# Kernel tuning notes

Hardware: AMD Instinct MI355X
Metric: run time of the kernel (lower is better)

Reference implementation:

```python
import jax, jax.numpy as jnp
import numpy as np


def gat(feat_src, feat_dst, src, dst, W, al, ar, b):
    # DGL GATConv in eval mode: shared fc for src/dst, additive attention,
    # leaky_relu(0.2), edge-softmax per destination node, elu activation, bias.
    H, D = al.shape
    nd = feat_dst.shape[0]
    hs = (feat_src @ W).reshape(-1, H, D)  # [Ns,H,D]
    hd = (feat_dst @ W).reshape(-1, H, D)  # [Nd,H,D]
    el = (hs * al).sum(-1)  # [Ns,H]
    er = (hd * ar).sum(-1)  # [Nd,H]
    e = jax.nn.leaky_relu(el[src] + er[dst], 0.2)  # [E,H]
    m = jax.lax.stop_gradient(jax.ops.segment_max(e, dst, num_segments=nd))
    a = jnp.exp(e - m[dst])
    s = jax.ops.segment_sum(a, dst, num_segments=nd)
    den = s[dst]
    alpha = a / jnp.where(den == 0, 1.0, den)  # allow_zero_in_degree
    rst = jax.ops.segment_sum(alpha[:, :, None] * hs[src], dst, num_segments=nd)
    return jax.nn.elu(rst + b.reshape(H, D))  # [Nd,H,D]


def setup_inputs():
    key = jax.random.key(0)
    ks = jax.random.split(key, 40)
    NP, NQ, NK, NA = 50000, 20000, 30000, 5000
    EM, EQ, EK, EA = 1600000, 200000, 200000, 100000
    IN, ATT, HID, H, OUT = 128, 64, 32, 4, 1000
    w = lambda k, sh: jax.random.normal(k, sh, jnp.float32) * 0.05
    ri = lambda k, e, n: jax.random.randint(k, (e,), 0, n, dtype=jnp.int32)
    d = dict(
        hp=jax.random.normal(ks[0], (NP, IN), jnp.float32),
        hq=jax.random.normal(ks[1], (NQ, ATT), jnp.float32),
        hk=jax.random.normal(ks[2], (NK, ATT), jnp.float32),
        ha=jax.random.normal(ks[3], (NA, ATT), jnp.float32),
        meta_src=ri(ks[4], EM, NP), meta_dst=ri(ks[5], EM, NP),
        q_src=ri(ks[6], EQ, NQ), q_dst=ri(ks[7], EQ, NP),
        k_src=ri(ks[8], EK, NK), k_dst=ri(ks[9], EK, NP),
        a_src=ri(ks[10], EA, NA), a_dst=ri(ks[11], EA, NP),
        W0=w(ks[12], (IN, H * HID)), al0=w(ks[13], (H, HID)), ar0=w(ks[14], (H, HID)), b0=jnp.zeros((H * HID,), jnp.float32),
        W1=w(ks[15], (H * HID, H * HID)), al1=w(ks[16], (H, HID)), ar1=w(ks[17], (H, HID)), b1=jnp.zeros((H * HID,), jnp.float32),
        Wq=w(ks[18], (64, H * 128)), alq=w(ks[19], (H, 128)), arq=w(ks[20], (H, 128)), bq=jnp.zeros((H * 128,), jnp.float32),
        Wkw=w(ks[21], (64, H * 128)), alkw=w(ks[22], (H, 128)), arkw=w(ks[23], (H, 128)), bkw=jnp.zeros((H * 128,), jnp.float32),
        Watt=w(ks[24], (64, H * 128)), alatt=w(ks[25], (H, 128)), aratt=w(ks[26], (H, 128)), batt=jnp.zeros((H * 128,), jnp.float32),
        Wpnn_a=w(ks[27], (IN, 64)), Wpn_a=w(ks[28], (ATT, 64)),
        Wpnn=w(ks[29], (H * HID, 64)), Wpn=w(ks[30], (H * 128, 64)),
        Wpred=w(ks[31], (256, OUT)), bpred=jnp.zeros((OUT,), jnp.float32),
    )
    return d


def reference(hp, hq, hk, ha, meta_src, meta_dst, q_src, q_dst, k_src, k_dst, a_src, a_dst, W0, al0, ar0, b0, W1, al1, ar1, b1, Wq, alq, arq, bq, Wkw, alkw, arkw, bkw, Watt, alatt, aratt, batt, Wpnn_a, Wpn_a, Wpnn, Wpn, Wpred, bpred):
    NP = hp.shape[0]
    # two pnn_layers over the single used metapath graph (index 1 is skipped in the original)
    h = gat(hp, hp, meta_src, meta_dst, W0, al0, ar0, b0).reshape(NP, -1)  # [NP,128]
    h = gat(h, h, meta_src, meta_dst, W1, al1, ar1, b1).reshape(NP, -1)    # [NP,128]
    hpd = hp @ Wpnn_a  # proj_pnn_a(hp_cache) -> dst features for bipartite GATs
    oq = gat(hq @ Wpn_a, hpd, q_src, q_dst, Wq, alq, arq, bq).reshape(NP, -1)      # [NP,512]
    ok = gat(hk @ Wpn_a, hpd, k_src, k_dst, Wkw, alkw, arkw, bkw).reshape(NP, -1)  # [NP,512]
    oa = gat(ha @ Wpn_a, hpd, a_src, a_dst, Watt, alatt, aratt, batt).reshape(NP, -1)  # [NP,512]
    hcat = jnp.concatenate([h @ Wpnn, oq @ Wpn, ok @ Wpn, oa @ Wpn], axis=1)  # [NP,256]
    return hcat @ Wpred + bpred
```

## Files before the change

### kernel.cpp

```cpp
#include <hip/hip_runtime.h>
#include <hip/hip_bf16.h>
#include <math.h>
#include <stdint.h>

typedef __attribute__((ext_vector_type(8))) short bh8;
typedef __attribute__((ext_vector_type(4))) float f32x4;

#define AS1(p) ((const __attribute__((address_space(1))) void*)(p))
#define AS3(p) ((__attribute__((address_space(3))) void*)(p))

__device__ inline ushort f2b(float f){
  uint u = __builtin_bit_cast(uint, f);
  u += 0x7fff + ((u >> 16) & 1);
  return (ushort)(u >> 16);
}
__device__ inline float b2f(ushort b){ return __builtin_bit_cast(float, (uint)b << 16); }

__global__ void fill_zero_i32(int* __restrict__ p, int n){
  int i = blockIdx.x*blockDim.x + threadIdx.x;
  if(i < n) p[i] = 0;
}

struct P4 { const int* src; const int* dst; uint* ebuf; int E; int cap; int bbeg; int bend; };

__global__ __launch_bounds__(256) void partition_all_k(P4 g0, P4 g1, P4 g2, P4 g3,
    int* __restrict__ bcur, int range){
  P4 G; int gi;
  int b = blockIdx.x;
  if(b < g0.bend){ G = g0; gi = 0; }
  else if(b < g1.bend){ G = g1; gi = 1; }
  else if(b < g2.bend){ G = g2; gi = 2; }
  else { G = g3; gi = 3; }
  const int lb = b - G.bbeg, nb = G.bend - G.bbeg;
  __shared__ int hist[8], base[8];
  const int tid = threadIdx.x;
  int* bc = bcur + gi*8;
  for(int c0 = lb*256; c0 < G.E; c0 += nb*256){
    int i = c0 + tid;
    int d = 0, s = 0, bk = -1;
    if(i < G.E){ d = G.dst[i]; s = G.src[i]; bk = d / range; }
    if(tid < 8) hist[tid] = 0;
    __syncthreads();
    int rank = 0;
    if(bk >= 0) rank = atomicAdd(&hist[bk], 1);
    __syncthreads();
    if(tid < 8) base[tid] = hist[tid] ? atomicAdd(&bc[tid], hist[tid]) : 0;
    __syncthreads();
    if(bk >= 0){
      int pos = base[bk] + rank;
      if(pos < G.cap) G.ebuf[(size_t)bk*G.cap + pos] = ((uint)s << 13) | (uint)(d - bk*range);
    }
    __syncthreads();
  }
}

struct B4 { const uint* ebuf; int cap; int* cnt; int bbeg; int bend; };
__global__ __launch_bounds__(256) void count_all_k(B4 g0, B4 g1, B4 g2, B4 g3,
    const int* __restrict__ bcur, int range){
  B4 G; int gi;
  int b = blockIdx.x;
  if(b < g0.bend){ G = g0; gi = 0; }
  else if(b < g1.bend){ G = g1; gi = 1; }
  else if(b < g2.bend){ G = g2; gi = 2; }
  else { G = g3; gi = 3; }
  const int local = b - G.bbeg, J = (G.bend - G.bbeg) >> 3;
  const int bk = local & 7, j = local >> 3;
  int nb = bcur[gi*8 + bk]; if(nb > G.cap) nb = G.cap;
  const uint* eb = G.ebuf + (size_t)bk*G.cap;
  int* cb = G.cnt + bk*range;
  int per = (nb + J - 1)/J;
  int beg = j*per, end = beg + per; if(end > nb) end = nb;
  for(int i = beg + threadIdx.x; i < end; i += 256)
    atomicAdd(&cb[eb[i] & 8191u], 1);
}

struct SB4 { const uint* ebuf; int cap; int* cursor; int* colv; int bbeg; int bend; };
__global__ __launch_bounds__(256) void scatter_all_k(SB4 g0, SB4 g1, SB4 g2, SB4 g3,
    const int* __restrict__ bcur, int range){
  SB4 G; int gi;
  int b = blockIdx.x;
  if(b < g0.bend){ G = g0; gi = 0; }
  else if(b < g1.bend){ G = g1; gi = 1; }
  else if(b < g2.bend){ G = g2; gi = 2; }
  else { G = g3; gi = 3; }
  const int local = b - G.bbeg, J = (G.bend - G.bbeg) >> 3;
  const int bk = local & 7, j = local >> 3;
  int nb = bcur[gi*8 + bk]; if(nb > G.cap) nb = G.cap;
  const uint* eb = G.ebuf + (size_t)bk*G.cap;
  int* ub = G.cursor + bk*range;
  int per = (nb + J - 1)/J;
  int beg = j*per, end = beg + per; if(end > nb) end = nb;
  for(int i = beg + threadIdx.x; i < end; i += 256){
    uint e = eb[i];
    int p = atomicAdd(&ub[e & 8191u], 1);
    G.colv[p] = (int)(e >> 13);
  }
}

__global__ __launch_bounds__(1024) void scan4_k(
    const int* c0, const int* c1, const int* c2, const int* c3,
    int* o0, int* o1, int* o2, int* o3,
    int* u0, int* u1, int* u2, int* u3, int n){
  const int* cnt = blockIdx.x==0?c0:(blockIdx.x==1?c1:(blockIdx.x==2?c2:c3));
  int* ofs    = blockIdx.x==0?o0:(blockIdx.x==1?o1:(blockIdx.x==2?o2:o3));
  int* cursor = blockIdx.x==0?u0:(blockIdx.x==1?u1:(blockIdx.x==2?u2:u3));
  __shared__ int wsum[16];
  __shared__ int carry_s;
  int tid = threadIdx.x, wid = tid >> 6, lane = tid & 63;
  if(tid == 0) carry_s = 0;
  __syncthreads();
  for(int base = 0; base < n; base += 4096){
    int i0 = base + tid*4;
    int4 v = make_int4(0,0,0,0);
    if(i0 + 3 < n) v = *(const int4*)(cnt + i0);
    else if(i0 < n){
      v.x = cnt[i0];
      if(i0+1 < n) v.y = cnt[i0+1];
      if(i0+2 < n) v.z = cnt[i0+2];
    }
    int s1 = v.x + v.y, s2 = s1 + v.z, tot = s2 + v.w;
    int x = tot;
    #pragma unroll
    for(int off = 1; off < 64; off <<= 1){
      int t = __shfl_up(x, off);
      if(lane >= off) x += t;
    }
    if(lane == 63) wsum[wid] = x;
    __syncthreads();
    if(tid < 16){
      int y = wsum[tid];
      #pragma unroll
      for(int off = 1; off < 16; off <<= 1){
        int t = __shfl_up(y, off);
        if(tid >= off) y += t;
      }
      wsum[tid] = y;
    }
    __syncthreads();
    int pre = (wid ? wsum[wid-1] : 0) + carry_s + (x - tot);
    if(i0 + 3 < n){
      int4 o = make_int4(pre, pre+v.x, pre+s1, pre+s2);
      *(int4*)(ofs + i0) = o;
      *(int4*)(cursor + i0) = o;
    } else if(i0 < n){
      ofs[i0] = pre; cursor[i0] = pre;
      if(i0+1 < n){ ofs[i0+1] = pre+v.x; cursor[i0+1] = pre+v.x; }
      if(i0+2 < n){ ofs[i0+2] = pre+s1; cursor[i0+2] = pre+s1; }
    }
    __syncthreads();
    if(tid == 0) carry_s += wsum[15];
    __syncthreads();
  }
  if(tid == 0) ofs[n] = carry_s;
}

__global__ void cvt_all_k(const float* i0, const float* i1, const float* i2, const float* i3,
    ushort* o0, ushort* o1, ushort* o2, ushort* o3, int4 cum){
  int i = blockIdx.x*blockDim.x + threadIdx.x;
  const float* in; ushort* out; int base;
  if(i < cum.x){ in=i0; out=o0; base=0; }
  else if(i < cum.y){ in=i1; out=o1; base=cum.x; }
  else if(i < cum.z){ in=i2; out=o2; base=cum.y; }
  else if(i < cum.w){ in=i3; out=o3; base=cum.z; }
  else return;
  int l = i - base;
  float4 v = ((const float4*)in)[l];
  ushort4 o; o.x=f2b(v.x); o.y=f2b(v.y); o.z=f2b(v.z); o.w=f2b(v.w);
  ((ushort4*)out)[l] = o;
}

struct WTD { const float* W; ushort* WT; int K; int N; };
struct WTAll { WTD d[7]; int cum[8]; };
__global__ void wT_all_k(WTAll a){
  int idx = blockIdx.x*blockDim.x + threadIdx.x;
  if(idx >= a.cum[7]) return;
  int j = 0;
  #pragma unroll
  for(int t = 1; t < 7; t++) if(idx >= a.cum[t]) j = t;
  int l = idx - a.cum[j];
  WTD d = a.d[j];
  int n = l / d.K, k = l - n*d.K;
  d.WT[l] = (n < d.N) ? f2b(d.W[(size_t)k*d.N + n]) : (ushort)0;
}

__global__ void wTg3_k(const float* W0, const float* W1, const float* W2, ushort* WT){
  int idx = blockIdx.x*blockDim.x + threadIdx.x;
  if(idx >= 3*32768) return;
  int g = idx >> 15, rem = idx & 32767;
  const float* W = g==0 ? W0 : (g==1 ? W1 : W2);
  int h = rem >> 13, r2 = rem & 8191;
  int n = r2 >> 6, k = r2 & 63;
  WT[idx] = f2b(W[(size_t)k*512 + h*128 + n]);
}

struct FD { const float* W; const float* a; float* out; int K; int D; };
struct FAll { FD d[10]; };
__global__ void fold_all_k(FAll f){
  FD d = f.d[blockIdx.x];
  for(int i = threadIdx.x; i < d.K*4; i += 256){
    int k = i >> 2, h = i & 3;
    const float* wr = d.W + (size_t)k*4*d.D + (size_t)h*d.D;
    const float* ar = d.a + (size_t)h*d.D;
    float s = 0.f;
    for(int dd = 0; dd < d.D; dd++) s += wr[dd]*ar[dd];
    d.out[i] = s;
  }
}

__device__ inline void ld4v(const float* p, float* v){
  float4 t = *(const float4*)p; v[0]=t.x; v[1]=t.y; v[2]=t.z; v[3]=t.w;
}
__device__ inline void ld4v(const ushort* p, float* v){
  ushort4 t = *(const ushort4*)p; v[0]=b2f(t.x); v[1]=b2f(t.y); v[2]=b2f(t.z); v[3]=b2f(t.w);
}

__global__ __launch_bounds__(256) void gemv4v_seg3(const ushort* __restrict__ A,
    const float* __restrict__ W0, const float* __restrict__ W1, const float* __restrict__ W2,
    float* __restrict__ outv, int M, int b1, int b2){
  const int w = (blockIdx.x*blockDim.x + threadIdx.x) >> 6;
  const int lane = threadIdx.x & 63;
  const int r = lane >> 4, q = lane & 15;
  int row = w*4 + r;
  bool valid = row < M;
  int rowc = valid ? row : (M-1);
  const float* Wf = rowc < b1 ? W0 : (rowc < b2 ? W1 : W2);
  float av[4];
  ld4v(A + (size_t)rowc*64 + q*4, av);
  float a[4] = {0.f,0.f,0.f,0.f};
  #pragma unroll
  for(int kk = 0; kk < 4; kk++){
    float4 wv = *(const float4*)(Wf + (q*4+kk)*4);
    a[0] += av[kk]*wv.x; a[1] += av[kk]*wv.y; a[2] += av[kk]*wv.z; a[3] += av[kk]*wv.w;
  }
  #pragma unroll
  for(int off = 1; off < 16; off <<= 1){
    a[0] += __shfl_xor(a[0], off); a[1] += __shfl_xor(a[1], off);
    a[2] += __shfl_xor(a[2], off); a[3] += __shfl_xor(a[3], off);
  }
  if(valid && q == 0){
    float4 o; o.x=a[0]; o.y=a[1]; o.z=a[2]; o.w=a[3];
    *(float4*)(outv + (size_t)row*4) = o;
  }
}

__global__ __launch_bounds__(256) void gemv4v_er3(const ushort* __restrict__ A,
    const float* __restrict__ W0, const float* __restrict__ W1, const float* __restrict__ W2,
    float* __restrict__ o0, float* __restrict__ o1, float* __restrict__ o2, int M){
  const int w = (blockIdx.x*blockDim.x + threadIdx.x) >> 6;
  const int lane = threadIdx.x & 63;
  const int r = lane >> 4, q = lane & 15;
  int row = w*4 + r;
  bool valid = row < M;
  int rowc = valid ? row : (M-1);
  float av[4];
  ld4v(A + (size_t)rowc*64 + q*4, av);
  float a[12];
  #pragma unroll
  for(int t = 0; t < 12; t++) a[t] = 0.f;
  #pragma unroll
  for(int kk = 0; kk < 4; kk++){
    float4 w0 = *(const float4*)(W0 + (q*4+kk)*4);
    float4 w1 = *(const float4*)(W1 + (q*4+kk)*4);
    float4 w2 = *(const float4*)(W2 + (q*4+kk)*4);
    a[0] += av[kk]*w0.x; a[1] += av[kk]*w0.y; a[2] += av[kk]*w0.z; a[3] += av[kk]*w0.w;
    a[4] += av[kk]*w1.x; a[5] += av[kk]*w1.y; a[6] += av[kk]*w1.z; a[7] += av[kk]*w1.w;
    a[8] += av[kk]*w2.x; a[9] += av[kk]*w2.y; a[10]+= av[kk]*w2.z; a[11]+= av[kk]*w2.w;
  }
  #pragma unroll
  for(int off = 1; off < 16; off <<= 1)
    #pragma unroll
    for(int t = 0; t < 12; t++) a[t] += __shfl_xor(a[t], off);
  if(valid && q == 0){
    float4 x; x.x=a[0]; x.y=a[1]; x.z=a[2]; x.w=a[3];
    *(float4*)(o0 + (size_t)row*4) = x;
    float4 y; y.x=a[4]; y.y=a[5]; y.z=a[6]; y.w=a[7];
    *(float4*)(o1 + (size_t)row*4) = y;
    float4 z; z.x=a[8]; z.y=a[9]; z.z=a[10]; z.w=a[11];
    *(float4*)(o2 + (size_t)row*4) = z;
  }
}

template<typename T>
__global__ __launch_bounds__(256) void gemv8v(const T* __restrict__ A,
    const float* __restrict__ Wfa, const float* __restrict__ Wfb,
    float* __restrict__ oa, float* __restrict__ ob, int M, int lda){
  const int w = (blockIdx.x*blockDim.x + threadIdx.x) >> 6;
  const int lane = threadIdx.x & 63;
  const int r = lane >> 5, q = lane & 31;
  int row = w*2 + r;
  bool valid = row < M;
  int rowc = valid ? row : (M-1);
  float av[4];
  ld4v(A + (size_t)rowc*lda + q*4, av);
  float a[4] = {0.f,0.f,0.f,0.f}, b[4] = {0.f,0.f,0.f,0.f};
  #pragma unroll
  for(int kk = 0; kk < 4; kk++){
    float4 wa = *(const float4*)(Wfa + (q*4+kk)*4);
    float4 wb = *(const float4*)(Wfb + (q*4+kk)*4);
    a[0] += av[kk]*wa.x; a[1] += av[kk]*wa.y; a[2] += av[kk]*wa.z; a[3] += av[kk]*wa.w;
    b[0] += av[kk]*wb.x; b[1] += av[kk]*wb.y; b[2] += av[kk]*wb.z; b[3] += av[kk]*wb.w;
  }
  #pragma unroll
  for(int off = 1; off < 32; off <<= 1){
    a[0] += __shfl_xor(a[0], off); a[1] += __shfl_xor(a[1], off);
    a[2] += __shfl_xor(a[2], off); a[3] += __shfl_xor(a[3], off);
    b[0] += __shfl_xor(b[0], off); b[1] += __shfl_xor(b[1], off);
    b[2] += __shfl_xor(b[2], off); b[3] += __shfl_xor(b[3], off);
  }
  if(valid && q == 0){
    float4 o; o.x=a[0]; o.y=a[1]; o.z=a[2]; o.w=a[3];
    *(float4*)(oa + (size_t)row*4) = o;
    float4 p; p.x=b[0]; p.y=b[1]; p.z=b[2]; p.w=b[3];
    *(float4*)(ob + (size_t)row*4) = p;
  }
}

struct GSeg { const ushort* A; const ushort* BT; const float* bias; void* C; int ldc; };

template<int BN, typename OutT, bool BIAS>
__global__ __launch_bounds__(256) void gemm_mfma_b(GSeg s0, GSeg s1, GSeg s2,
    int M, int N, int K, int lda){
  constexpr int BM = 128, BK = 64;
  constexpr int NI = BN/32;
  constexpr int AIT = BM*BK/(256*8);
  constexpr int BIT = BN*BK/(256*8);
  __shared__ ushort lds[BM*BK + BN*BK];
  ushort* ldsA = lds;
  ushort* ldsB = lds + BM*BK;
  GSeg S = blockIdx.z == 0 ? s0 : (blockIdx.z == 1 ? s1 : s2);
  const int tid = threadIdx.x, wid = tid >> 6, lane = tid & 63;
  const int wr = wid >> 1, wc = wid & 1;
  const int rowbase = blockIdx.x*BM;
  const int colbase = blockIdx.y*BN;

  f32x4 acc[4][NI];
  #pragma unroll
  for(int mi = 0; mi < 4; mi++)
    #pragma unroll
    for(int ni = 0; ni < NI; ni++) acc[mi][ni] = (f32x4)0.f;

  for(int k0 = 0; k0 < K; k0 += BK){
    #pragma unroll
    for(int it = 0; it < AIT; it++){
      int idx = it*256 + wid*64 + lane;
      int r = idx >> 3, sl = idx & 7;
      int kb = sl ^ (r & 7);
      int grow = rowbase + r; if(grow >= M) grow = M-1;
      const ushort* src = S.A + (size_t)grow*lda + k0 + kb*8;
      __builtin_amdgcn_global_load_lds(AS1(src), AS3(ldsA + (size_t)(it*256 + wid*64)*8), 16, 0, 0);
    }
    #pragma unroll
    for(int it = 0; it < BIT; it++){
      int idx = it*256 + wid*64 + lane;
      int r = idx >> 3, sl = idx & 7;
      int kb = sl ^ (r & 7);
      const ushort* src = S.BT + (size_t)(colbase + r)*K + k0 + kb*8;
      __builtin_amdgcn_global_load_lds(AS1(src), AS3(ldsB + (size_t)(it*256 + wid*64)*8), 16, 0, 0);
    }
    __syncthreads();
    #pragma unroll
    for(int kk = 0; kk < 2; kk++){
      bh8 af[4], bf[NI];
      #pragma unroll
      for(int mi = 0; mi < 4; mi++){
        int arow = wr*64 + mi*16 + (lane & 15);
        int kb = kk*4 + (lane >> 4);
        af[mi] = *(const bh8*)(ldsA + arow*BK + ((kb ^ (arow & 7)) << 3));
      }
      #pragma unroll
      for(int ni = 0; ni < NI; ni++){
        int brow = wc*(BN/2) + ni*16 + (lane & 15);
        int kb = kk*4 + (lane >> 4);
        bf[ni] = *(const bh8*)(ldsB + brow*BK + ((kb ^ (brow & 7)) << 3));
      }
      #pragma unroll
      for(int mi = 0; mi < 4; mi++)
        #pragma unroll
        for(int ni = 0; ni < NI; ni++)
          acc[mi][ni] = __builtin_amdgcn_mfma_f32_16x16x32_bf16(af[mi], bf[ni], acc[mi][ni], 0, 0, 0);
    }
    __syncthreads();
  }
  OutT* C = (OutT*)S.C;
  #pragma unroll
  for(int mi = 0; mi < 4; mi++){
    #pragma unroll
    for(int ni = 0; ni < NI; ni++){
      int col = colbase + wc*(BN/2) + ni*16 + (lane & 15);
      if(col >= N) continue;
      float bv = BIAS ? S.bias[col] : 0.f;
      #pragma unroll
      for(int j = 0; j < 4; j++){
        int row = rowbase + wr*64 + mi*16 + (lane >> 4)*4 + j;
        if(row >= M) continue;
        float v = acc[mi][ni][j] + bv;
        if constexpr (sizeof(OutT) == 4) C[(size_t)row*S.ldc + col] = v;
        else                             C[(size_t)row*S.ldc + col] = (OutT)f2b(v);
      }
    }
  }
}

__global__ __launch_bounds__(256) void bip_tail_k(
    const ushort* __restrict__ agg,
    const ushort* __restrict__ WTg3,
    const ushort* __restrict__ WpnT,
    const float* bias0, const float* bias1, const float* bias2,
    ushort* __restrict__ hcat,
    int M){
  __shared__ ushort ldsA[128*64];
  __shared__ ushort ldsB[128*64];
  __shared__ ushort ldsP[128*128];
  __shared__ ushort ldsW[64*128];
  const int seg = blockIdx.z;
  const ushort* A  = agg + (size_t)seg*M*256;
  const ushort* Wg = WTg3 + (size_t)seg*32768;
  const float* bias = seg==0 ? bias0 : (seg==1 ? bias1 : bias2);
  ushort* outp = hcat + 64 + seg*64;
  const int tid = threadIdx.x, lane = tid & 63, wid = tid >> 6;
  const int wr = wid >> 1, wc = wid & 1;
  const int rowbase = blockIdx.x*128;

  f32x4 acc_out[4][2];
  #pragma unroll
  for(int mi = 0; mi < 4; mi++){ acc_out[mi][0] = (f32x4)0.f; acc_out[mi][1] = (f32x4)0.f; }

  for(int hh = 0; hh < 4; hh++){
    #pragma unroll
    for(int it = 0; it < 4; it++){
      int idx = it*256 + tid;
      int r = idx >> 3, sl = idx & 7;
      int kb = sl ^ (r & 7);
      int grow = rowbase + r; if(grow >= M) grow = M-1;
      __builtin_amdgcn_global_load_lds(AS1(A + (size_t)grow*256 + hh*64 + kb*8),
                                       AS3(ldsA + (size_t)idx*8), 16, 0, 0);
    }
    #pragma unroll
    for(int it = 0; it < 4; it++){
      int idx = it*256 + tid;
      int r = idx >> 3, sl = idx & 7;
      int kb = sl ^ (r & 7);
      __builtin_amdgcn_global_load_lds(AS1(Wg + hh*8192 + r*64 + kb*8),
                                       AS3(ldsB + (size_t)idx*8), 16, 0, 0);
    }
    #pragma unroll
    for(int it = 0; it < 4; it++){
      int idx = it*256 + tid;
      int r = idx >> 4, sl = idx & 15;
      int kb = sl ^ (r & 7);
      __builtin_amdgcn_global_load_lds(AS1(WpnT + (size_t)r*512 + hh*128 + kb*8),
                                       AS3(ldsW + (size_t)idx*8), 16, 0, 0);
    }
    __syncthreads();
    f32x4 accp[4][4];
    #pragma unroll
    for(int mi = 0; mi < 4; mi++)
      #pragma unroll
      for(int ni = 0; ni < 4; ni++) accp[mi][ni] = (f32x4)0.f;
    #pragma unroll
    for(int kk = 0; kk < 2; kk++){
      bh8 af[4], bf[4];
      int kb = kk*4 + (lane >> 4);
      #pragma unroll
      for(int mi = 0; mi < 4; mi++){
        int arow = wr*64 + mi*16 + (lane & 15);
        af[mi] = *(const bh8*)(ldsA + arow*64 + ((kb ^ (arow & 7)) << 3));
      }
      #pragma unroll
      for(int ni = 0; ni < 4; ni++){
        int brow = wc*64 + ni*16 + (lane & 15);
        bf[ni] = *(const bh8*)(ldsB + brow*64 + ((kb ^ (brow & 7)) << 3));
      }
      #pragma unroll
      for(int mi = 0; mi < 4; mi++)
        #pragma unroll
        for(int ni = 0; ni < 4; ni++)
          accp[mi][ni] = __builtin_amdgcn_mfma_f32_16x16x32_bf16(af[mi], bf[ni], accp[mi][ni], 0, 0, 0);
    }
    #pragma unroll
    for(int mi = 0; mi < 4; mi++)
      #pragma unroll
      for(int ni = 0; ni < 4; ni++){
        int col = wc*64 + ni*16 + (lane & 15);
        float bv = bias[hh*128 + col];
        int rbase = wr*64 + mi*16 + (lane >> 4)*4;
        #pragma unroll
        for(int j = 0; j < 4; j++){
          float v = accp[mi][ni][j] + bv;
          v = v > 0.f ? v : (__expf(v) - 1.f);
          int row = rbase + j;
          ldsP[row*128 + ((((col >> 3) ^ (row & 7))) << 3) + (col & 7)] = f2b(v);
        }
      }
    __syncthreads();
    #pragma unroll
    for(int kk = 0; kk < 4; kk++){
      bh8 af[4], bf[2];
      int kb = kk*4 + (lane >> 4);
      #pragma unroll
      for(int mi = 0; mi < 4; mi++){
        int arow = wr*64 + mi*16 + (lane & 15);
        af[mi] = *(const bh8*)(ldsP + arow*128 + ((kb ^ (arow & 7)) << 3));
      }
      #pragma unroll
      for(int ni = 0; ni < 2; ni++){
        int brow = wc*32 + ni*16 + (lane & 15);
        bf[ni] = *(const bh8*)(ldsW + brow*128 + ((kb ^ (brow & 7)) << 3));
      }
      #pragma unroll
      for(int mi = 0; mi < 4; mi++)
        #pragma unroll
        for(int ni = 0; ni < 2; ni++)
          acc_out[mi][ni] = __builtin_amdgcn_mfma_f32_16x16x32_bf16(af[mi], bf[ni], acc_out[mi][ni], 0, 0, 0);
    }
    __syncthreads();
  }
  #pragma unroll
  for(int mi = 0; mi < 4; mi++)
    #pragma unroll
    for(int ni = 0; ni < 2; ni++){
      int col = wc*32 + ni*16 + (lane & 15);
      #pragma unroll
      for(int j = 0; j < 4; j++){
        int row = rowbase + wr*64 + mi*16 + (lane >> 4)*4 + j;
        if(row >= M) continue;
        outp[(size_t)row*256 + col] = f2b(acc_out[mi][ni][j]);
      }
    }
}

__global__ __launch_bounds__(256) void gat_agg_meta(
    const ushort* __restrict__ hs, const float* __restrict__ el,
    const float* __restrict__ er, const int* __restrict__ ofs,
    const int* __restrict__ colv, const float* __restrict__ bias,
    ushort* __restrict__ outv, int Nd){
  const int wslot = threadIdx.x >> 6;
  const int node = blockIdx.x*4 + wslot;
  const int lane = threadIdx.x & 63;
  __shared__ int   lds_s[4][64];
  __shared__ float lds_w[4][256];
  if(node >= Nd) return;
  const int e0 = ofs[node], e1 = ofs[node+1];
  const int g = lane >> 4, q = lane & 15;
  const int hh = q >> 2;
  const float4 erv = *(const float4*)(er + (size_t)node*4);
  float m0=-INFINITY, m1=-INFINITY, m2=-INFINITY, m3=-INFINITY;
  float sw0=0.f, sw1=0.f, sw2=0.f, sw3=0.f;
  float acc[8];
  #pragma unroll
  for(int r = 0; r < 8; r++) acc[r] = 0.f;

  for(int base = e0; base < e1; base += 64){
    int nch = e1 - base; if(nch > 64) nch = 64;
    int s_l = colv[base + (lane < nch ? lane : nch-1)];
    float4 ev = *(const float4*)(el + (size_t)s_l*4);
    float x0 = ev.x + erv.x; x0 = x0 > 0.f ? x0 : 0.2f*x0;
    float x1 = ev.y + erv.y; x1 = x1 > 0.f ? x1 : 0.2f*x1;
    float x2 = ev.z + erv.z; x2 = x2 > 0.f ? x2 : 0.2f*x2;
    float x3 = ev.w + erv.w; x3 = x3 > 0.f ? x3 : 0.2f*x3;
    if(lane >= nch){ x0 = x1 = x2 = x3 = -INFINITY; }
    float c0=x0, c1=x1, c2=x2, c3=x3;
    #pragma unroll
    for(int off = 32; off; off >>= 1){
      c0 = fmaxf(c0, __shfl_xor(c0, off));
      c1 = fmaxf(c1, __shfl_xor(c1, off));
      c2 = fmaxf(c2, __shfl_xor(c2, off));
      c3 = fmaxf(c3, __shfl_xor(c3, off));
    }
    float n0 = fmaxf(m0,c0), n1 = fmaxf(m1,c1), n2 = fmaxf(m2,c2), n3 = fmaxf(m3,c3);
    float r0 = __expf(m0-n0), r1 = __expf(m1-n1), r2 = __expf(m2-n2), r3 = __expf(m3-n3);
    float w0 = __expf(x0-n0), w1 = __expf(x1-n1), w2 = __expf(x2-n2), w3 = __expf(x3-n3);
    sw0 = sw0*r0 + w0; sw1 = sw1*r1 + w1; sw2 = sw2*r2 + w2; sw3 = sw3*r3 + w3;
    float rh = hh==0 ? r0 : (hh==1 ? r1 : (hh==2 ? r2 : r3));
    #pragma unroll
    for(int r = 0; r < 8; r++) acc[r] *= rh;
    m0=n0; m1=n1; m2=n2; m3=n3;
    lds_s[wslot][lane] = s_l;
    lds_w[wslot][lane*4+0] = w0; lds_w[wslot][lane*4+1] = w1;
    lds_w[wslot][lane*4+2] = w2; lds_w[wslot][lane*4+3] = w3;
    int npad = (nch + 7) & ~7;
    for(int j = 0; j < npad; j += 8){
      int sA = lds_s[wslot][j + g];
      int sB = lds_s[wslot][j + 4 + g];
      float wA = lds_w[wslot][(j + g)*4 + hh];
      float wB = lds_w[wslot][(j + 4 + g)*4 + hh];
      bh8 vA = *(const bh8*)(hs + (size_t)sA*128 + q*8);
      bh8 vB = *(const bh8*)(hs + (size_t)sB*128 + q*8);
      #pragma unroll
      for(int r = 0; r < 8; r++) acc[r] += wA * b2f((ushort)vA[r]);
      #pragma unroll
      for(int r = 0; r < 8; r++) acc[r] += wB * b2f((ushort)vB[r]);
    }
  }
  #pragma unroll
  for(int off = 32; off; off >>= 1){
    sw0 += __shfl_xor(sw0, off); sw1 += __shfl_xor(sw1, off);
    sw2 += __shfl_xor(sw2, off); sw3 += __shfl_xor(sw3, off);
  }
  #pragma unroll
  for(int r = 0; r < 8; r++){
    acc[r] += __shfl_xor(acc[r], 16);
    acc[r] += __shfl_xor(acc[r], 32);
  }
  float swh = hh==0 ? sw0 : (hh==1 ? sw1 : (hh==2 ? sw2 : sw3));
  float den = (swh == 0.f) ? 1.f : swh;
  if(g == 0){
    bh8 ov;
    #pragma unroll
    for(int r = 0; r < 8; r++){
      float v = acc[r]/den + bias[q*8 + r];
      v = v > 0.f ? v : (__expf(v) - 1.f);
      ov[r] = (short)f2b(v);
    }
    *(bh8*)(outv + (size_t)node*128 + q*8) = ov;
  }
}

struct ASeg { const int* ofs; const int* colv; const float* el; const float* er; ushort* agg; };
__global__ __launch_bounds__(256) void gat_agg_proj3(ASeg s0, ASeg s1, ASeg s2,
    const ushort* __restrict__ proj, int2 pbase, int Nd, int nb){
  const int seg = blockIdx.x / nb;
  const ASeg S = seg == 0 ? s0 : (seg == 1 ? s1 : s2);
  const ushort* pj = proj + (size_t)(seg == 0 ? 0 : (seg == 1 ? pbase.x : pbase.y))*64;
  const int node = (blockIdx.x - seg*nb)*16 + (threadIdx.x >> 4);
  const int q = threadIdx.x & 15;
  if(node >= Nd) return;
  const int e0 = S.ofs[node], e1 = S.ofs[node+1];
  const float4 erv = *(const float4*)(S.er + (size_t)node*4);
  float m0=-INFINITY, m1=-INFINITY, m2=-INFINITY, m3=-INFINITY;
  for(int e = e0; e < e1; e++){
    int s = S.colv[e];
    float4 ev = *(const float4*)(S.el + (size_t)s*4);
    float x0 = ev.x + erv.x; x0 = x0 > 0.f ? x0 : 0.2f*x0;
    float x1 = ev.y + erv.y; x1 = x1 > 0.f ? x1 : 0.2f*x1;
    float x2 = ev.z + erv.z; x2 = x2 > 0.f ? x2 : 0.2f*x2;
    float x3 = ev.w + erv.w; x3 = x3 > 0.f ? x3 : 0.2f*x3;
    m0 = fmaxf(m0,x0); m1 = fmaxf(m1,x1); m2 = fmaxf(m2,x2); m3 = fmaxf(m3,x3);
  }
  float sw0=0.f, sw1=0.f, sw2=0.f, sw3=0.f;
  float acc[4][4];
  #pragma unroll
  for(int d = 0; d < 4; d++)
    #pragma unroll
    for(int h = 0; h < 4; h++) acc[d][h] = 0.f;
  for(int e = e0; e < e1; e++){
    int s = S.colv[e];
    float4 ev = *(const float4*)(S.el + (size_t)s*4);
    float x0 = ev.x + erv.x; x0 = x0 > 0.f ? x0 : 0.2f*x0;
    float x1 = ev.y + erv.y; x1 = x1 > 0.f ? x1 : 0.2f*x1;
    float x2 = ev.z + erv.z; x2 = x2 > 0.f ? x2 : 0.2f*x2;
    float x3 = ev.w + erv.w; x3 = x3 > 0.f ? x3 : 0.2f*x3;
    float w0 = __expf(x0-m0), w1 = __expf(x1-m1);
    float w2 = __expf(x2-m2), w3 = __expf(x3-m3);
    sw0 += w0; sw1 += w1; sw2 += w2; sw3 += w3;
    ushort4 p = *(const ushort4*)(pj + (size_t)s*64 + q*4);
    float f0 = b2f(p.x), f1 = b2f(p.y), f2 = b2f(p.z), f3 = b2f(p.w);
    acc[0][0] += w0*f0; acc[0][1] += w1*f0; acc[0][2] += w2*f0; acc[0][3] += w3*f0;
    acc[1][0] += w0*f1; acc[1][1] += w1*f1; acc[1][2] += w2*f1; acc[1][3] += w3*f1;
    acc[2][0] += w0*f2; acc[2][1] += w1*f2; acc[2][2] += w2*f2; acc[2][3] += w3*f2;
    acc[3][0] += w0*f3; acc[3][1] += w1*f3; acc[3][2] += w2*f3; acc[3][3] += w3*f3;
  }
  float dn[4];
  dn[0] = (sw0 == 0.f) ? 1.f : sw0;
  dn[1] = (sw1 == 0.f) ? 1.f : sw1;
  dn[2] = (sw2 == 0.f) ? 1.f : sw2;
  dn[3] = (sw3 == 0.f) ? 1.f : sw3;
  ushort* orow = S.agg + (size_t)node*256;
  #pragma unroll
  for(int h = 0; h < 4; h++){
    ushort4 o;
    o.x = f2b(acc[0][h]/dn[h]); o.y = f2b(acc[1][h]/dn[h]);
    o.z = f2b(acc[2][h]/dn[h]); o.w = f2b(acc[3][h]/dn[h]);
    *(ushort4*)(orow + h*64 + q*4) = o;
  }
}

extern "C" void kernel_launch(void* const* d_in, const int* in_sizes, int n_in,
                              void* d_out, int out_size, void* d_ws, size_t ws_size,
                              hipStream_t stream){
  const float* hp   = (const float*)d_in[0];
  const float* hq   = (const float*)d_in[1];
  const float* hk   = (const float*)d_in[2];
  const float* ha   = (const float*)d_in[3];
  const int* meta_src = (const int*)d_in[4];
  const int* meta_dst = (const int*)d_in[5];
  const int* q_src = (const int*)d_in[6];
  const int* q_dst = (const int*)d_in[7];
  const int* k_src = (const int*)d_in[8];
  const int* k_dst = (const int*)d_in[9];
  const int* a_src = (const int*)d_in[10];
  const int* a_dst = (const int*)d_in[11];
  const float* W0  = (const float*)d_in[12]; const float* al0 = (const float*)d_in[13];
  const float* ar0 = (const float*)d_in[14]; const float* b0  = (const float*)d_in[15];
  const float* W1  = (const float*)d_in[16]; const float* al1 = (const float*)d_in[17];
  const float* ar1 = (const float*)d_in[18]; const float* b1  = (const float*)d_in[19];
  const float* Wq  = (const float*)d_in[20]; const float* alq = (const float*)d_in[21];
  const float* arq = (const float*)d_in[22]; const float* bq  = (const float*)d_in[23];
  const float* Wkw = (const float*)d_in[24]; const float* alkw= (const float*)d_in[25];
  const float* arkw= (const float*)d_in[26]; const float* bkw = (const float*)d_in[27];
  const float* Watt= (const float*)d_in[28]; const float* alatt=(const float*)d_in[29];
  const float* aratt=(const float*)d_in[30]; const float* batt= (const float*)d_in[31];
  const float* Wpnn_a = (const float*)d_in[32];
  const float* Wpn_a  = (const float*)d_in[33];
  const float* Wpnn   = (const float*)d_in[34];
  const float* Wpn    = (const float*)d_in[35];
  const float* Wpred  = (const float*)d_in[36];
  const float* bpred  = (const float*)d_in[37];
  (void)n_in; (void)out_size; (void)ws_size;

  const int IN = 128, ATT = 64;
  const int NP = in_sizes[0]/IN, NQ = in_sizes[1]/ATT, NK = in_sizes[2]/ATT, NA = in_sizes[3]/ATT;
  const int EM = in_sizes[4], EQ = in_sizes[6], EK = in_sizes[8], EA = in_sizes[10];
  const int range = (NP + 7)/8;
  const int NS = NQ + NK + NA;

  uint8_t* wp = (uint8_t*)d_ws;
  auto alloc = [&](size_t bytes)->uint8_t*{
    uint8_t* p = wp; wp += (bytes + 255) & ~(size_t)255; return p;
  };
  ushort* hcat_b = (ushort*)alloc((size_t)NP*256*2);
  ushort* hbuf_b = (ushort*)alloc((size_t)NP*128*2);
  ushort* hp_b   = (ushort*)alloc((size_t)NP*128*2);
  ushort* hpd_b  = (ushort*)alloc((size_t)NP*64*2);
  ushort* hs_b   = (ushort*)alloc((size_t)NP*128*2);
  ushort* feat_all = (ushort*)alloc((size_t)NS*64*2);
  ushort* proj_all = (ushort*)alloc((size_t)NS*64*2);
  ushort* agg_all  = (ushort*)alloc((size_t)3*NP*256*2);
  float* el    = (float*)alloc((size_t)NP*4*4);
  float* er    = (float*)alloc((size_t)NP*4*4);
  float* el_all= (float*)alloc((size_t)NS*4*4);
  float* er_all= (float*)alloc((size_t)3*NP*4*4);
  float* wf    = (float*)alloc((size_t)10*512*4);
  int* cnt4    = (int*)alloc((size_t)(4*NP+32)*4);
  int* bcur    = cnt4 + 4*NP;
  int* cur4    = (int*)alloc((size_t)4*NP*4);
  int* ofsm    = (int*)alloc((size_t)(NP+4)*4);
  int* ofsq    = (int*)alloc((size_t)(NP+4)*4);
  int* ofsk    = (int*)alloc((size_t)(NP+4)*4);
  int* ofsa    = (int*)alloc((size_t)(NP+4)*4);
  int* colm    = (int*)alloc((size_t)EM*4);
  int* colq    = (int*)alloc((size_t)EQ*4);
  int* colk    = (int*)alloc((size_t)EK*4);
  int* cola    = (int*)alloc((size_t)EA*4);
  const int capM = EM/4+1024, capQ = EQ/4+1024, capK = EK/4+1024, capA = EA/4+1024;
  uint* ebm = (uint*)alloc((size_t)8*capM*4);
  uint* ebq = (uint*)alloc((size_t)8*capQ*4);
  uint* ebk = (uint*)alloc((size_t)8*capK*4);
  uint* eba = (uint*)alloc((size_t)8*capA*4);
  ushort* W0T    = (ushort*)alloc(128*128*2);
  ushort* W1T    = (ushort*)alloc(128*128*2);
  ushort* WTg3   = (ushort*)alloc((size_t)3*4*128*64*2);
  ushort* WpnT   = (ushort*)alloc((size_t)64*512*2);
  ushort* WpnnT  = (ushort*)alloc(64*128*2);
  ushort* Wpnn_aT= (ushort*)alloc(64*128*2);
  ushort* Wpn_aT = (ushort*)alloc(64*64*2);
  ushort* WpredT = (ushort*)alloc((size_t)1024*256*2);

  fill_zero_i32<<<(4*NP+32+255)/256, 256, 0, stream>>>(cnt4, 4*NP+32);
  {
    int bm = EM/1024 + 1, bq2 = EQ/1024 + 1, bk2 = EK/1024 + 1, ba2 = EA/1024 + 1;
    P4 g0{meta_src, meta_dst, ebm, EM, capM, 0, bm};
    P4 g1{q_src, q_dst, ebq, EQ, capQ, bm, bm+bq2};
    P4 g2{k_src, k_dst, ebk, EK, capK, bm+bq2, bm+bq2+bk2};
    P4 g3{a_src, a_dst, eba, EA, capA, bm+bq2+bk2, bm+bq2+bk2+ba2};
    partition_all_k<<<g3.bend, 256, 0, stream>>>(g0, g1, g2, g3, bcur, range);
  }
  auto Jof = [&](int E){ int J = E/65536 + 8; if(J > 48) J = 48; return J; };
  {
    int jm = 8*Jof(EM), jq = 8*Jof(EQ), jk = 8*Jof(EK), ja = 8*Jof(EA);
    B4 g0{ebm, capM, cnt4 + 0*NP, 0, jm};
    B4 g1{ebq, capQ, cnt4 + 1*NP, jm, jm+jq};
    B4 g2{ebk, capK, cnt4 + 2*NP, jm+jq, jm+jq+jk};
    B4 g3{eba, capA, cnt4 + 3*NP, jm+jq+jk, jm+jq+jk+ja};
    count_all_k<<<g3.bend, 256, 0, stream>>>(g0, g1, g2, g3, bcur, range);
    scan4_k<<<4, 1024, 0, stream>>>(cnt4, cnt4+NP, cnt4+2*NP, cnt4+3*NP,
                                    ofsm, ofsq, ofsk, ofsa,
                                    cur4, cur4+NP, cur4+2*NP, cur4+3*NP, NP);
    SB4 s0{ebm, capM, cur4 + 0*NP, colm, 0, jm};
    SB4 s1{ebq, capQ, cur4 + 1*NP, colq, jm, jm+jq};
    SB4 s2{ebk, capK, cur4 + 2*NP, colk, jm+jq, jm+jq+jk};
    SB4 s3{eba, capA, cur4 + 3*NP, cola, jm+jq+jk, jm+jq+jk+ja};
    scatter_all_k<<<s3.bend, 256, 0, stream>>>(s0, s1, s2, s3, bcur, range);
  }

  {
    int c0 = NP*128/4, c1 = c0 + NQ*64/4, c2 = c1 + NK*64/4, c3 = c2 + NA*64/4;
    cvt_all_k<<<(c3+255)/256, 256, 0, stream>>>(hp, hq, hk, ha,
        hp_b, feat_all, feat_all + (size_t)NQ*64, feat_all + (size_t)(NQ+NK)*64,
        make_int4(c0, c1, c2, c3));
  }
  {
    WTAll a;
    a.d[0] = {W0, W0T, 128, 128};      a.d[1] = {W1, W1T, 128, 128};
    a.d[2] = {Wpn, WpnT, 512, 64};     a.d[3] = {Wpnn, WpnnT, 128, 64};
    a.d[4] = {Wpnn_a, Wpnn_aT, 128, 64}; a.d[5] = {Wpn_a, Wpn_aT, 64, 64};
    a.d[6] = {Wpred, WpredT, 256, 1000};
    int items[7] = {128*128, 128*128, 64*512, 64*128, 64*128, 64*64, 1024*256};
    a.cum[0] = 0;
    for(int t = 0; t < 7; t++) a.cum[t+1] = a.cum[t] + items[t];
    wT_all_k<<<(a.cum[7]+255)/256, 256, 0, stream>>>(a);
  }
  wTg3_k<<<(3*32768+255)/256, 256, 0, stream>>>(Wq, Wkw, Watt, WTg3);
  {
    FAll f;
    f.d[0] = {W0, al0, wf+0*512, 128, 32};  f.d[1] = {W0, ar0, wf+1*512, 128, 32};
    f.d[2] = {W1, al1, wf+2*512, 128, 32};  f.d[3] = {W1, ar1, wf+3*512, 128, 32};
    f.d[4] = {Wq, alq, wf+4*512, 64, 128};  f.d[5] = {Wq, arq, wf+5*512, 64, 128};
    f.d[6] = {Wkw, alkw, wf+6*512, 64, 128};f.d[7] = {Wkw, arkw, wf+7*512, 64, 128};
    f.d[8] = {Watt, alatt, wf+8*512, 64, 128};f.d[9] = {Watt, aratt, wf+9*512, 64, 128};
    fold_all_k<<<10, 256, 0, stream>>>(f);
  }

  auto launch_gemm = [&]<int BN, typename OutT, bool BIAS>(
      GSeg a, GSeg b, GSeg c, int nseg, int M, int N, int K, int lda){
    int Npad = (N + BN - 1)/BN*BN;
    dim3 g((M + 127)/128, Npad/BN, nseg);
    gemm_mfma_b<BN, OutT, BIAS><<<g, 256, 0, stream>>>(a, b, c, M, N, K, lda);
  };
  GSeg z{};

  launch_gemm.template operator()<128, ushort, false>(
      GSeg{hp_b, W0T, nullptr, hs_b, 128}, z, z, 1, NP, 128, 128, 128);
  gemv8v<ushort><<<(NP/2+3)/4, 256, 0, stream>>>(hp_b, wf+0*512, wf+1*512, el, er, NP, 128);
  gat_agg_meta<<<(NP+3)/4, 256, 0, stream>>>(hs_b, el, er, ofsm, colm, b0, hbuf_b, NP);

  launch_gemm.template operator()<128, ushort, false>(
      GSeg{hbuf_b, W1T, nullptr, hs_b, 128}, z, z, 1, NP, 128, 128, 128);
  gemv8v<ushort><<<(NP/2+3)/4, 256, 0, stream>>>(hbuf_b, wf+2*512, wf+3*512, el, er, NP, 128);
  gat_agg_meta<<<(NP+3)/4, 256, 0, stream>>>(hs_b, el, er, ofsm, colm, b1, hbuf_b, NP);

  launch_gemm.template operator()<64, ushort, false>(
      GSeg{hbuf_b, WpnnT, nullptr, hcat_b, 256},
      GSeg{hp_b, Wpnn_aT, nullptr, hpd_b, 64}, z, 2, NP, 64, 128, 128);

  launch_gemm.template operator()<64, ushort, false>(
      GSeg{feat_all, Wpn_aT, nullptr, proj_all, 64}, z, z, 1, NS, 64, 64, 64);
  gemv4v_seg3<<<(NS/4+3)/4, 256, 0, stream>>>(proj_all, wf+4*512, wf+6*512, wf+8*512,
      el_all, NS, NQ, NQ+NK);
  gemv4v_er3<<<(NP/4+3)/4, 256, 0, stream>>>(hpd_b, wf+5*512, wf+7*512, wf+9*512,
      er_all, er_all + (size_t)NP*4, er_all + (size_t)2*NP*4, NP);
  {
    int nb = (NP+15)/16;
    ASeg a0{ofsq, colq, el_all,                    er_all,                    agg_all};
    ASeg a1{ofsk, colk, el_all + (size_t)NQ*4,     er_all + (size_t)NP*4,     agg_all + (size_t)NP*256};
    ASeg a2{ofsa, cola, el_all + (size_t)(NQ+NK)*4,er_all + (size_t)2*NP*4,   agg_all + (size_t)2*NP*256};
    gat_agg_proj3<<<3*nb, 256, 0, stream>>>(a0, a1, a2, proj_all, make_int2(NQ, NQ+NK), NP, nb);
  }
  {
    dim3 g((NP+127)/128, 1, 3);
    bip_tail_k<<<g, 256, 0, stream>>>(agg_all, WTg3, WpnT, bq, bkw, batt, hcat_b, NP);
  }

  launch_gemm.template operator()<128, float, true>(
      GSeg{hcat_b, WpredT, bpred, d_out, 1000}, z, z, 1, NP, 1000, 256, 256);
}
```

Measured before the change: 805.4 us.

## Fuse degree counting into partition and unroll edge-gather loops

Degree counting moves into the partition kernel as a global atomic per edge, so the separate count kernel and its second pass over the bucket buffers go away. The metapath aggregation loop now issues four neighbour-row loads per iteration instead of two, exposing more memory-level parallelism. The bipartite aggregation kernel gains a fast path for nodes with degree up to 8. That path loads all indices and features up front and computes max and softmax in registers instead of walking the edge list twice. The cost is scattered global atomics in partition, which may contend, plus higher register pressure.

```diff
diff --git a/kernel.cpp b/kernel.cpp
--- a/kernel.cpp
+++ b/kernel.cpp
@@ -21,7 +21,7 @@
   if(i < n) p[i] = 0;
 }
 
-struct P4 { const int* src; const int* dst; uint* ebuf; int E; int cap; int bbeg; int bend; };
+struct P4 { const int* src; const int* dst; uint* ebuf; int* cnt; int E; int cap; int bbeg; int bend; };
 
 __global__ __launch_bounds__(256) void partition_all_k(P4 g0, P4 g1, P4 g2, P4 g3,
     int* __restrict__ bcur, int range){
@@ -42,7 +42,10 @@
     if(tid < 8) hist[tid] = 0;
     __syncthreads();
     int rank = 0;
-    if(bk >= 0) rank = atomicAdd(&hist[bk], 1);
+    if(bk >= 0){
+      rank = atomicAdd(&hist[bk], 1);
+      atomicAdd(&G.cnt[d], 1);
+    }
     __syncthreads();
     if(tid < 8) base[tid] = hist[tid] ? atomicAdd(&bc[tid], hist[tid]) : 0;
     __syncthreads();
@@ -52,26 +55,6 @@
     }
     __syncthreads();
   }
-}
-
-struct B4 { const uint* ebuf; int cap; int* cnt; int bbeg; int bend; };
-__global__ __launch_bounds__(256) void count_all_k(B4 g0, B4 g1, B4 g2, B4 g3,
-    const int* __restrict__ bcur, int range){
-  B4 G; int gi;
-  int b = blockIdx.x;
-  if(b < g0.bend){ G = g0; gi = 0; }
-  else if(b < g1.bend){ G = g1; gi = 1; }
-  else if(b < g2.bend){ G = g2; gi = 2; }
-  else { G = g3; gi = 3; }
-  const int local = b - G.bbeg, J = (G.bend - G.bbeg) >> 3;
-  const int bk = local & 7, j = local >> 3;
-  int nb = bcur[gi*8 + bk]; if(nb > G.cap) nb = G.cap;
-  const uint* eb = G.ebuf + (size_t)bk*G.cap;
-  int* cb = G.cnt + bk*range;
-  int per = (nb + J - 1)/J;
-  int beg = j*per, end = beg + per; if(end > nb) end = nb;
-  for(int i = beg + threadIdx.x; i < end; i += 256)
-    atomicAdd(&cb[eb[i] & 8191u], 1);
 }
 
 struct SB4 { const uint* ebuf; int cap; int* cursor; int* colv; int bbeg; int bend; };
@@ -578,18 +561,22 @@
     lds_s[wslot][lane] = s_l;
     lds_w[wslot][lane*4+0] = w0; lds_w[wslot][lane*4+1] = w1;
     lds_w[wslot][lane*4+2] = w2; lds_w[wslot][lane*4+3] = w3;
-    int npad = (nch + 7) & ~7;
-    for(int j = 0; j < npad; j += 8){
-      int sA = lds_s[wslot][j + g];
-      int sB = lds_s[wslot][j + 4 + g];
-      float wA = lds_w[wslot][(j + g)*4 + hh];
-      float wB = lds_w[wslot][(j + 4 + g)*4 + hh];
-      bh8 vA = *(const bh8*)(hs + (size_t)sA*128 + q*8);
-      bh8 vB = *(const bh8*)(hs + (size_t)sB*128 + q*8);
-      #pragma unroll
-      for(int r = 0; r < 8; r++) acc[r] += wA * b2f((ushort)vA[r]);
-      #pragma unroll
-      for(int r = 0; r < 8; r++) acc[r] += wB * b2f((ushort)vB[r]);
+    int npad = (nch + 15) & ~15;
+    for(int j = 0; j < npad; j += 16){
+      int sv[4]; float wv[4];
+      #pragma unroll
+      for(int u = 0; u < 4; u++){
+        sv[u] = lds_s[wslot][j + u*4 + g];
+        wv[u] = lds_w[wslot][(j + u*4 + g)*4 + hh];
+      }
+      bh8 vv[4];
+      #pragma unroll
+      for(int u = 0; u < 4; u++)
+        vv[u] = *(const bh8*)(hs + (size_t)sv[u]*128 + q*8);
+      #pragma unroll
+      for(int u = 0; u < 4; u++)
+        #pragma unroll
+        for(int r = 0; r < 8; r++) acc[r] += wv[u] * b2f((ushort)vv[u][r]);
     }
   }
   #pragma unroll
@@ -626,39 +613,77 @@
   const int q = threadIdx.x & 15;
   if(node >= Nd) return;
   const int e0 = S.ofs[node], e1 = S.ofs[node+1];
+  const int deg = e1 - e0;
   const float4 erv = *(const float4*)(S.er + (size_t)node*4);
-  float m0=-INFINITY, m1=-INFINITY, m2=-INFINITY, m3=-INFINITY;
-  for(int e = e0; e < e1; e++){
-    int s = S.colv[e];
-    float4 ev = *(const float4*)(S.el + (size_t)s*4);
-    float x0 = ev.x + erv.x; x0 = x0 > 0.f ? x0 : 0.2f*x0;
-    float x1 = ev.y + erv.y; x1 = x1 > 0.f ? x1 : 0.2f*x1;
-    float x2 = ev.z + erv.z; x2 = x2 > 0.f ? x2 : 0.2f*x2;
-    float x3 = ev.w + erv.w; x3 = x3 > 0.f ? x3 : 0.2f*x3;
-    m0 = fmaxf(m0,x0); m1 = fmaxf(m1,x1); m2 = fmaxf(m2,x2); m3 = fmaxf(m3,x3);
-  }
   float sw0=0.f, sw1=0.f, sw2=0.f, sw3=0.f;
   float acc[4][4];
   #pragma unroll
   for(int d = 0; d < 4; d++)
     #pragma unroll
     for(int h = 0; h < 4; h++) acc[d][h] = 0.f;
-  for(int e = e0; e < e1; e++){
-    int s = S.colv[e];
-    float4 ev = *(const float4*)(S.el + (size_t)s*4);
-    float x0 = ev.x + erv.x; x0 = x0 > 0.f ? x0 : 0.2f*x0;
-    float x1 = ev.y + erv.y; x1 = x1 > 0.f ? x1 : 0.2f*x1;
-    float x2 = ev.z + erv.z; x2 = x2 > 0.f ? x2 : 0.2f*x2;
-    float x3 = ev.w + erv.w; x3 = x3 > 0.f ? x3 : 0.2f*x3;
-    float w0 = __expf(x0-m0), w1 = __expf(x1-m1);
-    float w2 = __expf(x2-m2), w3 = __expf(x3-m3);
-    sw0 += w0; sw1 += w1; sw2 += w2; sw3 += w3;
-    ushort4 p = *(const ushort4*)(pj + (size_t)s*64 + q*4);
-    float f0 = b2f(p.x), f1 = b2f(p.y), f2 = b2f(p.z), f3 = b2f(p.w);
-    acc[0][0] += w0*f0; acc[0][1] += w1*f0; acc[0][2] += w2*f0; acc[0][3] += w3*f0;
-    acc[1][0] += w0*f1; acc[1][1] += w1*f1; acc[1][2] += w2*f1; acc[1][3] += w3*f1;
-    acc[2][0] += w0*f2; acc[2][1] += w1*f2; acc[2][2] += w2*f2; acc[2][3] += w3*f2;
-    acc[3][0] += w0*f3; acc[3][1] += w1*f3; acc[3][2] += w2*f3; acc[3][3] += w3*f3;
+
+  if(deg <= 8){
+    const int ebase = (deg > 0) ? e0 : 0;
+    int sv[8];
+    #pragma unroll
+    for(int u = 0; u < 8; u++) sv[u] = S.colv[ebase + (u < deg ? u : 0)];
+    float xa[8], xb[8], xc[8], xd[8];
+    #pragma unroll
+    for(int u = 0; u < 8; u++){
+      float4 ev = *(const float4*)(S.el + (size_t)sv[u]*4);
+      float t0 = ev.x + erv.x; xa[u] = t0 > 0.f ? t0 : 0.2f*t0;
+      float t1 = ev.y + erv.y; xb[u] = t1 > 0.f ? t1 : 0.2f*t1;
+      float t2 = ev.z + erv.z; xc[u] = t2 > 0.f ? t2 : 0.2f*t2;
+      float t3 = ev.w + erv.w; xd[u] = t3 > 0.f ? t3 : 0.2f*t3;
+    }
+    float m0=-INFINITY, m1=-INFINITY, m2=-INFINITY, m3=-INFINITY;
+    #pragma unroll
+    for(int u = 0; u < 8; u++) if(u < deg){
+      m0 = fmaxf(m0, xa[u]); m1 = fmaxf(m1, xb[u]);
+      m2 = fmaxf(m2, xc[u]); m3 = fmaxf(m3, xd[u]);
+    }
+    ushort4 pv[8];
+    #pragma unroll
+    for(int u = 0; u < 8; u++) pv[u] = *(const ushort4*)(pj + (size_t)sv[u]*64 + q*4);
+    #pragma unroll
+    for(int u = 0; u < 8; u++) if(u < deg){
+      float w0 = __expf(xa[u]-m0), w1 = __expf(xb[u]-m1);
+      float w2 = __expf(xc[u]-m2), w3 = __expf(xd[u]-m3);
+      sw0 += w0; sw1 += w1; sw2 += w2; sw3 += w3;
+      float f0 = b2f(pv[u].x), f1 = b2f(pv[u].y), f2 = b2f(pv[u].z), f3 = b2f(pv[u].w);
+      acc[0][0] += w0*f0; acc[0][1] += w1*f0; acc[0][2] += w2*f0; acc[0][3] += w3*f0;
+      acc[1][0] += w0*f1; acc[1][1] += w1*f1; acc[1][2] += w2*f1; acc[1][3] += w3*f1;
+      acc[2][0] += w0*f2; acc[2][1] += w1*f2; acc[2][2] += w2*f2; acc[2][3] += w3*f2;
+      acc[3][0] += w0*f3; acc[3][1] += w1*f3; acc[3][2] += w2*f3; acc[3][3] += w3*f3;
+    }
+  } else {
+    float m0=-INFINITY, m1=-INFINITY, m2=-INFINITY, m3=-INFINITY;
+    for(int e = e0; e < e1; e++){
+      int s = S.colv[e];
+      float4 ev = *(const float4*)(S.el + (size_t)s*4);
+      float x0 = ev.x + erv.x; x0 = x0 > 0.f ? x0 : 0.2f*x0;
+      float x1 = ev.y + erv.y; x1 = x1 > 0.f ? x1 : 0.2f*x1;
+      float x2 = ev.z + erv.z; x2 = x2 > 0.f ? x2 : 0.2f*x2;
+      float x3 = ev.w + erv.w; x3 = x3 > 0.f ? x3 : 0.2f*x3;
+      m0 = fmaxf(m0,x0); m1 = fmaxf(m1,x1); m2 = fmaxf(m2,x2); m3 = fmaxf(m3,x3);
+    }
+    for(int e = e0; e < e1; e++){
+      int s = S.colv[e];
+      float4 ev = *(const float4*)(S.el + (size_t)s*4);
+      float x0 = ev.x + erv.x; x0 = x0 > 0.f ? x0 : 0.2f*x0;
+      float x1 = ev.y + erv.y; x1 = x1 > 0.f ? x1 : 0.2f*x1;
+      float x2 = ev.z + erv.z; x2 = x2 > 0.f ? x2 : 0.2f*x2;
+      float x3 = ev.w + erv.w; x3 = x3 > 0.f ? x3 : 0.2f*x3;
+      float w0 = __expf(x0-m0), w1 = __expf(x1-m1);
+      float w2 = __expf(x2-m2), w3 = __expf(x3-m3);
+      sw0 += w0; sw1 += w1; sw2 += w2; sw3 += w3;
+      ushort4 p = *(const ushort4*)(pj + (size_t)s*64 + q*4);
+      float f0 = b2f(p.x), f1 = b2f(p.y), f2 = b2f(p.z), f3 = b2f(p.w);
+      acc[0][0] += w0*f0; acc[0][1] += w1*f0; acc[0][2] += w2*f0; acc[0][3] += w3*f0;
+      acc[1][0] += w0*f1; acc[1][1] += w1*f1; acc[1][2] += w2*f1; acc[1][3] += w3*f1;
+      acc[2][0] += w0*f2; acc[2][1] += w1*f2; acc[2][2] += w2*f2; acc[2][3] += w3*f2;
+      acc[3][0] += w0*f3; acc[3][1] += w1*f3; acc[3][2] += w2*f3; acc[3][3] += w3*f3;
+    }
   }
   float dn[4];
   dn[0] = (sw0 == 0.f) ? 1.f : sw0;
@@ -759,23 +784,18 @@
   fill_zero_i32<<<(4*NP+32+255)/256, 256, 0, stream>>>(cnt4, 4*NP+32);
   {
     int bm = EM/1024 + 1, bq2 = EQ/1024 + 1, bk2 = EK/1024 + 1, ba2 = EA/1024 + 1;
-    P4 g0{meta_src, meta_dst, ebm, EM, capM, 0, bm};
-    P4 g1{q_src, q_dst, ebq, EQ, capQ, bm, bm+bq2};
-    P4 g2{k_src, k_dst, ebk, EK, capK, bm+bq2, bm+bq2+bk2};
-    P4 g3{a_src, a_dst, eba, EA, capA, bm+bq2+bk2, bm+bq2+bk2+ba2};
+    P4 g0{meta_src, meta_dst, ebm, cnt4 + 0*NP, EM, capM, 0, bm};
+    P4 g1{q_src, q_dst, ebq, cnt4 + 1*NP, EQ, capQ, bm, bm+bq2};
+    P4 g2{k_src, k_dst, ebk, cnt4 + 2*NP, EK, capK, bm+bq2, bm+bq2+bk2};
+    P4 g3{a_src, a_dst, eba, cnt4 + 3*NP, EA, capA, bm+bq2+bk2, bm+bq2+bk2+ba2};
     partition_all_k<<<g3.bend, 256, 0, stream>>>(g0, g1, g2, g3, bcur, range);
   }
   auto Jof = [&](int E){ int J = E/65536 + 8; if(J > 48) J = 48; return J; };
   {
-    int jm = 8*Jof(EM), jq = 8*Jof(EQ), jk = 8*Jof(EK), ja = 8*Jof(EA);
-    B4 g0{ebm, capM, cnt4 + 0*NP, 0, jm};
-    B4 g1{ebq, capQ, cnt4 + 1*NP, jm, jm+jq};
-    B4 g2{ebk, capK, cnt4 + 2*NP, jm+jq, jm+jq+jk};
-    B4 g3{eba, capA, cnt4 + 3*NP, jm+jq+jk, jm+jq+jk+ja};
-    count_all_k<<<g3.bend, 256, 0, stream>>>(g0, g1, g2, g3, bcur, range);
     scan4_k<<<4, 1024, 0, stream>>>(cnt4, cnt4+NP, cnt4+2*NP, cnt4+3*NP,
                                     ofsm, ofsq, ofsk, ofsa,
                                     cur4, cur4+NP, cur4+2*NP, cur4+3*NP, NP);
+    int jm = 8*Jof(EM), jq = 8*Jof(EQ), jk = 8*Jof(EK), ja = 8*Jof(EA);
     SB4 s0{ebm, capM, cur4 + 0*NP, colm, 0, jm};
     SB4 s1{ebq, capQ, cur4 + 1*NP, colq, jm, jm+jq};
     SB4 s2{ebk, capK, cur4 + 2*NP, colk, jm+jq, jm+jq+jk};
```

Result: faster. 758.2 us (-5.9%).
